# Performance work log

Measured on AMD Instinct MI355X. Metric: run time of the kernel, lower is better.

The kernel has to match this reference:

```python
import jax, jax.numpy as jnp
import numpy as np
import math

EMBED = 1024
HEADS = 16
HEAD_DIM = EMBED // HEADS


def setup_inputs() -> dict:
    key = jax.random.key(0)
    ks = jax.random.split(key, 6)
    scale = 1.0 / math.sqrt(EMBED)
    x = jax.random.normal(ks[0], (4, 2048, EMBED), dtype=jnp.float32)
    Wv = jax.random.normal(ks[1], (EMBED, EMBED), dtype=jnp.float32) * scale
    Wk = jax.random.normal(ks[2], (EMBED, EMBED), dtype=jnp.float32) * scale
    Wq = jax.random.normal(ks[3], (EMBED, EMBED), dtype=jnp.float32) * scale
    Wo = jax.random.normal(ks[4], (EMBED, EMBED), dtype=jnp.float32) * scale
    bo = jax.random.normal(ks[5], (EMBED,), dtype=jnp.float32) * 0.02
    return {"x": x, "Wq": Wq, "Wk": Wk, "Wv": Wv, "Wo": Wo, "bo": bo}


def reference(x, Wq, Wk, Wv, Wo, bo):
    N, S, E = x.shape
    H, D = HEADS, HEAD_DIM
    # Linear(E,E,bias=False): y = x @ W.T ; weights here stored as [out,in]
    q = (x @ Wq.T).reshape(N, S, H, D)
    k = (x @ Wk.T).reshape(N, S, H, D)
    v = (x @ Wv.T).reshape(N, S, H, D)
    energy = jnp.einsum('nqhd,nkhd->nhqk', q, k)  # [N,H,S,S]
    attn = jax.nn.softmax(energy / math.sqrt(D), axis=-1)
    out = jnp.einsum('nhql,nlhd->nqhd', attn, v).reshape(N, S, E)
    return out @ Wo.T + bo
```

## Files before the change

kernel.cpp:

```cpp
#include <hip/hip_runtime.h>
#include <stdint.h>

#define NB   4
#define SLEN 2048
#define EMB  1024
#define NH   16
#define HD   64
#define MTOT (NB * SLEN)

typedef __bf16 bf8_t  __attribute__((ext_vector_type(8)));
typedef __bf16 bf4_t  __attribute__((ext_vector_type(4)));
typedef float  f4_t   __attribute__((ext_vector_type(4)));
typedef unsigned int u32x2 __attribute__((ext_vector_type(2)));
typedef unsigned int u32x4 __attribute__((ext_vector_type(4)));

#if __has_builtin(__builtin_amdgcn_exp2f)
#define EXP2(x) __builtin_amdgcn_exp2f(x)
#else
#define EXP2(x) exp2f(x)
#endif

__device__ __forceinline__ void gld16(const void* g, void* l) {
    __builtin_amdgcn_global_load_lds(
        (__attribute__((address_space(1))) void*)(g),
        (__attribute__((address_space(3))) void*)(l),
        16, 0, 0);
}

__device__ __forceinline__ uint32_t pack_bf16_rtn(float a, float b) {
    uint32_t ua = __builtin_bit_cast(uint32_t, a) + 0x8000u;
    uint32_t ub = __builtin_bit_cast(uint32_t, b) + 0x8000u;
    return __builtin_amdgcn_perm(ub, ua, 0x07060302u);
}
__device__ __forceinline__ uint32_t pack_bf16_rtz(float a, float b) {
    return __builtin_amdgcn_perm(__builtin_bit_cast(uint32_t, b),
                                 __builtin_bit_cast(uint32_t, a), 0x07060302u);
}

__global__ __launch_bounds__(256) void cast_all(const float* __restrict__ x,
                                                const float* __restrict__ Wq,
                                                const float* __restrict__ Wk,
                                                const float* __restrict__ Wv,
                                                const float* __restrict__ Wo,
                                                __bf16* __restrict__ xb,
                                                __bf16* __restrict__ wb) {
    int b = blockIdx.x;
    const float* s;
    __bf16* d;
    if (b < 8192) {
        s = x; d = xb;
    } else {
        int y = (b - 8192) >> 10;
        s = (y == 0) ? Wq : (y == 1) ? Wk : (y == 2) ? Wv : Wo;
        d = wb + (size_t)y * (EMB * EMB);
        b = (b - 8192) & 1023;
    }
    int i = (b * 256 + (int)threadIdx.x) * 4;
    float4 f = *(const float4*)(s + i);
    bf4_t o = { (__bf16)f.x, (__bf16)f.y, (__bf16)f.z, (__bf16)f.w };
    *(bf4_t*)(d + i) = o;
}

__device__ __forceinline__ void gstage(const __bf16* __restrict__ A,
                                       const __bf16* __restrict__ B,
                                       int m0, int n0, int k0, int K, int tid,
                                       __bf16* __restrict__ As,
                                       __bf16* __restrict__ Bs) {
#pragma unroll
    for (int t = 0; t < 4; ++t) {
        int c   = t * 256 + tid;
        int row = c >> 3;
        int kc  = (c & 7) ^ (row & 7);
        int cb  = c & ~63;
        gld16(A + (size_t)(m0 + row) * K + k0 + kc * 8, As + cb * 8);
        gld16(B + (size_t)(n0 + row) * K + k0 + kc * 8, Bs + cb * 8);
    }
}

template <bool SWAP>
__device__ __forceinline__ void gcompute(const __bf16* __restrict__ As,
                                         const __bf16* __restrict__ Bs,
                                         f4_t (*acc)[4],
                                         int wm, int wn, int quad, int l16) {
#pragma unroll
    for (int ks = 0; ks < 2; ++ks) {
        bf8_t af[4], bfr[4];
#pragma unroll
        for (int i = 0; i < 4; ++i) {
            int r = wm + i * 16 + l16;
            af[i] = *(const bf8_t*)&As[r * 64 + (((ks * 4 + quad) ^ (r & 7)) * 8)];
        }
#pragma unroll
        for (int j = 0; j < 4; ++j) {
            int r = wn + j * 16 + l16;
            bfr[j] = *(const bf8_t*)&Bs[r * 64 + (((ks * 4 + quad) ^ (r & 7)) * 8)];
        }
#pragma unroll
        for (int i = 0; i < 4; ++i)
#pragma unroll
            for (int j = 0; j < 4; ++j) {
                if (SWAP)
                    acc[i][j] = __builtin_amdgcn_mfma_f32_16x16x32_bf16(
                        bfr[j], af[i], acc[i][j], 0, 0, 0);
                else
                    acc[i][j] = __builtin_amdgcn_mfma_f32_16x16x32_bf16(
                        af[i], bfr[j], acc[i][j], 0, 0, 0);
            }
    }
}

template <bool SWAP>
__device__ __forceinline__ void gkloop(const __bf16* __restrict__ A,
                                       const __bf16* __restrict__ B,
                                       int m0, int n0, int K, int tid,
                                       __bf16* As0, __bf16* Bs0,
                                       __bf16* As1, __bf16* Bs1,
                                       f4_t (*acc)[4],
                                       int wm, int wn, int quad, int l16) {
    gstage(A, B, m0, n0, 0, K, tid, As0, Bs0);
    for (int k0 = 0; k0 < K; k0 += 128) {
        __syncthreads();
        gstage(A, B, m0, n0, k0 + 64, K, tid, As1, Bs1);
        gcompute<SWAP>(As0, Bs0, acc, wm, wn, quad, l16);
        __syncthreads();
        int knn = (k0 + 128 < K) ? k0 + 128 : k0 + 64;
        gstage(A, B, m0, n0, knn, K, tid, As0, Bs0);
        gcompute<SWAP>(As1, Bs1, acc, wm, wn, quad, l16);
    }
}

__global__ __launch_bounds__(256, 2) void proj_qkv(const __bf16* __restrict__ A,
                                                   const __bf16* __restrict__ B,
                                                   __bf16* __restrict__ qb) {
    __shared__ __bf16 As0[128 * 64], Bs0[128 * 64];
    __shared__ __bf16 As1[128 * 64], Bs1[128 * 64];

    const int tid  = threadIdx.x;
    const int lane = tid & 63;
    const int w    = tid >> 6;
    const int quad = lane >> 4;
    const int l16  = lane & 15;
    const int m0   = blockIdx.x * 128;
    const int n0   = blockIdx.y * 128;
    const int wm   = (w >> 1) * 64;
    const int wn   = (w & 1) * 64;

    f4_t acc[4][4];
#pragma unroll
    for (int i = 0; i < 4; ++i)
#pragma unroll
        for (int j = 0; j < 4; ++j) acc[i][j] = (f4_t){0.f, 0.f, 0.f, 0.f};

    if (n0 < 2048) {
        gkloop<true>(A, B, m0, n0, EMB, tid, As0, Bs0, As1, Bs1, acc, wm, wn, quad, l16);
#pragma unroll
        for (int i = 0; i < 4; ++i)
#pragma unroll
            for (int j = 0; j < 4; ++j) {
                int m   = m0 + wm + i * 16 + l16;
                int col = n0 + wn + j * 16 + quad * 4;
                __bf16* dst = (col < 1024) ? qb : qb + (size_t)8 * 1024 * 1024;
                bf4_t pk = { (__bf16)acc[i][j][0], (__bf16)acc[i][j][1],
                             (__bf16)acc[i][j][2], (__bf16)acc[i][j][3] };
                *(bf4_t*)&dst[(size_t)m * 1024 + (col & 1023)] = pk;
            }
    } else {
        gkloop<false>(A, B, m0, n0, EMB, tid, As0, Bs0, As1, Bs1, acc, wm, wn, quad, l16);
        __bf16* vtb = qb + (size_t)16 * 1024 * 1024;
#pragma unroll
        for (int i = 0; i < 4; ++i)
#pragma unroll
            for (int j = 0; j < 4; ++j) {
                int m  = m0 + wm + i * 16 + quad * 4;
                int ch = n0 - 2048 + wn + j * 16 + l16;
                size_t idx = ((size_t)(m >> 11) * 1024 + ch) * 2048 + (m & 2047);
                bf4_t pk = { (__bf16)acc[i][j][0], (__bf16)acc[i][j][1],
                             (__bf16)acc[i][j][2], (__bf16)acc[i][j][3] };
                *(bf4_t*)&vtb[idx] = pk;
            }
    }
}

__global__ __launch_bounds__(256, 2) void gemm_out(const __bf16* __restrict__ A,
                                                   const __bf16* __restrict__ B,
                                                   float* __restrict__ C,
                                                   const float* __restrict__ bias) {
    __shared__ __bf16 As0[128 * 64], Bs0[128 * 64];
    __shared__ __bf16 As1[128 * 64], Bs1[128 * 64];

    const int tid  = threadIdx.x;
    const int lane = tid & 63;
    const int w    = tid >> 6;
    const int quad = lane >> 4;
    const int l16  = lane & 15;
    const int m0   = blockIdx.x * 128;
    const int n0   = blockIdx.y * 128;
    const int wm   = (w >> 1) * 64;
    const int wn   = (w & 1) * 64;

    f4_t acc[4][4];
#pragma unroll
    for (int i = 0; i < 4; ++i)
#pragma unroll
        for (int j = 0; j < 4; ++j) acc[i][j] = (f4_t){0.f, 0.f, 0.f, 0.f};

    gkloop<true>(A, B, m0, n0, EMB, tid, As0, Bs0, As1, Bs1, acc, wm, wn, quad, l16);

#pragma unroll
    for (int i = 0; i < 4; ++i)
#pragma unroll
        for (int j = 0; j < 4; ++j) {
            int m   = m0 + wm + i * 16 + l16;
            int col = n0 + wn + j * 16 + quad * 4;
            float4 bv = *(const float4*)&bias[col];
            float4 ov = { acc[i][j][0] + bv.x, acc[i][j][1] + bv.y,
                          acc[i][j][2] + bv.z, acc[i][j][3] + bv.w };
            *(float4*)&C[(size_t)m * EMB + col] = ov;
        }
}

__device__ __forceinline__ void attn_stage(const __bf16* __restrict__ kbase,
                                           const __bf16* __restrict__ vbase,
                                           int l0, int tid,
                                           __bf16* __restrict__ Ksb,
                                           __bf16* __restrict__ Vsb) {
    int c   = tid;
    int row = c >> 3;
    int kc  = (c & 7) ^ (row & 7);
    int cb  = c & ~63;
    gld16(kbase + (size_t)(l0 + row) * EMB + kc * 8, Ksb + cb * 8);
    gld16(vbase + (size_t)row * SLEN + l0 + kc * 8, Vsb + cb * 8);
}

__device__ __forceinline__ void attn_tile(const __bf16* __restrict__ Ksb,
                                          const __bf16* __restrict__ Vsb,
                                          const bf8_t (*bq)[2], bf8_t aones,
                                          f4_t* ls, f4_t (*o)[4],
                                          int quad, int l16, int sw) {
#pragma unroll
    for (int ks = 0; ks < 2; ++ks) {
        uint32_t pk[2][4];
#pragma unroll
        for (int jkl = 0; jkl < 2; ++jkl) {
            const int jk = ks * 2 + jkl;
            bf8_t ak0 = *(const bf8_t*)&Ksb[(jk * 16 + l16) * 64 + ((quad ^ sw) * 8)];
            bf8_t ak1 = *(const bf8_t*)&Ksb[(jk * 16 + l16) * 64 + (((4 + quad) ^ sw) * 8)];
#pragma unroll
            for (int jq = 0; jq < 2; ++jq) {
                f4_t e = (f4_t){0.f, 0.f, 0.f, 0.f};
                e = __builtin_amdgcn_mfma_f32_16x16x32_bf16(ak0, bq[jq][0], e, 0, 0, 0);
                e = __builtin_amdgcn_mfma_f32_16x16x32_bf16(ak1, bq[jq][1], e, 0, 0, 0);
                pk[jq][jkl * 2 + 0] = pack_bf16_rtz(EXP2(e[0]), EXP2(e[1]));
                pk[jq][jkl * 2 + 1] = pack_bf16_rtz(EXP2(e[2]), EXP2(e[3]));
            }
        }
        bf8_t bp[2];
#pragma unroll
        for (int jq = 0; jq < 2; ++jq) {
            u32x2 s0 = __builtin_amdgcn_permlane32_swap(pk[jq][0], pk[jq][2], false, false);
            u32x2 s1 = __builtin_amdgcn_permlane32_swap(pk[jq][1], pk[jq][3], false, false);
            u32x2 t0 = __builtin_amdgcn_permlane16_swap(s0[0], s0[1], false, false);
            u32x2 t1 = __builtin_amdgcn_permlane16_swap(s1[0], s1[1], false, false);
            bp[jq] = __builtin_bit_cast(bf8_t, (u32x4){t0[0], t1[0], t0[1], t1[1]});
        }
#pragma unroll
        for (int jq = 0; jq < 2; ++jq)
            ls[jq] = __builtin_amdgcn_mfma_f32_16x16x32_bf16(aones, bp[jq], ls[jq], 0, 0, 0);
#pragma unroll
        for (int jd = 0; jd < 4; ++jd) {
            bf8_t av = *(const bf8_t*)&Vsb[(jd * 16 + l16) * 64 +
                                           (((ks * 4 + quad) ^ sw) * 8)];
#pragma unroll
            for (int jq = 0; jq < 2; ++jq)
                o[jq][jd] = __builtin_amdgcn_mfma_f32_16x16x32_bf16(av, bp[jq],
                                                                    o[jq][jd], 0, 0, 0);
        }
    }
}

__global__ __launch_bounds__(512, 4) void attn_fwd(const __bf16* __restrict__ Q,
                                                   const __bf16* __restrict__ K,
                                                   const __bf16* __restrict__ Vt,
                                                   __bf16* __restrict__ O) {
    __shared__ __bf16 Ks0[64 * 64];
    __shared__ __bf16 Ks1[64 * 64];
    __shared__ __bf16 Vs0[64 * 64];
    __shared__ __bf16 Vs1[64 * 64];

    const int tid  = threadIdx.x;
    const int lane = tid & 63;
    const int w    = tid >> 6;
    const int quad = lane >> 4;
    const int l16  = lane & 15;
    const int nh   = blockIdx.x;
    const int n    = nh >> 4;
    const int h    = nh & 15;
    const int q0   = blockIdx.y * 256 + w * 32;

    const float QSCALE = 0.125f * 1.44269504f;

    bf8_t bq[2][2];
#pragma unroll
    for (int jq = 0; jq < 2; ++jq)
#pragma unroll
        for (int ks = 0; ks < 2; ++ks) {
            bf8_t v = *(const bf8_t*)(Q + (size_t)(n * SLEN + q0 + jq * 16 + l16) * EMB +
                                      h * HD + ks * 32 + quad * 8);
#pragma unroll
            for (int t = 0; t < 8; ++t) v[t] = (__bf16)((float)v[t] * QSCALE);
            bq[jq][ks] = v;
        }

    bf8_t aones;
#pragma unroll
    for (int t = 0; t < 8; ++t) aones[t] = (__bf16)1.0f;

    f4_t ls[2];
    f4_t o[2][4];
#pragma unroll
    for (int jq = 0; jq < 2; ++jq) {
        ls[jq] = (f4_t){0.f, 0.f, 0.f, 0.f};
#pragma unroll
        for (int jd = 0; jd < 4; ++jd) o[jq][jd] = (f4_t){0.f, 0.f, 0.f, 0.f};
    }

    const __bf16* kbase = K + (size_t)n * SLEN * EMB + h * HD;
    const __bf16* vbase = Vt + (size_t)nh * HD * SLEN;
    const int sw = l16 & 7;

    attn_stage(kbase, vbase, 0, tid, Ks0, Vs0);

    for (int it = 0; it < 32; it += 2) {
        int l0 = it * 64;
        __syncthreads();
        attn_stage(kbase, vbase, l0 + 64, tid, Ks1, Vs1);
        attn_tile(Ks0, Vs0, bq, aones, ls, o, quad, l16, sw);
        __syncthreads();
        int lnn = (l0 + 128 < SLEN) ? l0 + 128 : l0 + 64;
        attn_stage(kbase, vbase, lnn, tid, Ks0, Vs0);
        attn_tile(Ks1, Vs1, bq, aones, ls, o, quad, l16, sw);
    }

#pragma unroll
    for (int jq = 0; jq < 2; ++jq) {
        float inv = 1.0f / ls[jq][0];
#pragma unroll
        for (int jd = 0; jd < 4; ++jd) {
            uint32_t d0 = pack_bf16_rtn(o[jq][jd][0] * inv, o[jq][jd][1] * inv);
            uint32_t d1 = pack_bf16_rtn(o[jq][jd][2] * inv, o[jq][jd][3] * inv);
            *(uint2*)&O[(size_t)(n * SLEN + q0 + jq * 16 + l16) * EMB + h * HD +
                        jd * 16 + quad * 4] = (uint2){d0, d1};
        }
    }
}

extern "C" void kernel_launch(void* const* d_in, const int* in_sizes, int n_in,
                              void* d_out, int out_size, void* d_ws, size_t ws_size,
                              hipStream_t stream) {
    const float* x  = (const float*)d_in[0];
    const float* Wq = (const float*)d_in[1];
    const float* Wk = (const float*)d_in[2];
    const float* Wv = (const float*)d_in[3];
    const float* Wo = (const float*)d_in[4];
    const float* bo = (const float*)d_in[5];

    char* wsb = (char*)d_ws;
    const size_t MB = (size_t)1 << 20;
    __bf16* xb  = (__bf16*)(wsb + 0 * MB);
    __bf16* ab  = xb;
    __bf16* wqb = (__bf16*)(wsb + 16 * MB);
    __bf16* wob = (__bf16*)(wsb + 22 * MB);
    __bf16* qb  = (__bf16*)(wsb + 24 * MB);
    __bf16* kb  = (__bf16*)(wsb + 40 * MB);
    __bf16* vtb = (__bf16*)(wsb + 56 * MB);

    cast_all<<<dim3(12288), dim3(256), 0, stream>>>(x, Wq, Wk, Wv, Wo, xb, wqb);

    proj_qkv<<<dim3(MTOT / 128, 3072 / 128), 256, 0, stream>>>(xb, wqb, qb);

    attn_fwd<<<dim3(NB * NH, SLEN / 256), 512, 0, stream>>>(qb, kb, vtb, ab);

    gemm_out<<<dim3(MTOT / 128, EMB / 128), 256, 0, stream>>>(ab, wob, (float*)d_out, bo);
}
```

Measured before the change: 241.4 us.

## Software-pipeline QK-exp and PV across paired KV tiles with double-sized stages

The attention inner loop now processes two 64-key tiles per stage and interleaves the QK/exp computation of the next half-tile with the PV MFMAs of the previous one. The goal is to hide exp/permlane latency behind matrix work. PV MFMAs run at raised wave priority via s_setprio. Shared memory doubles to four K/V buffers, which lowers how many blocks fit per CU and raises register pressure from the extra live pk arrays. The final prefetch wraps back to tile 0 to avoid an out-of-range load.

```diff
diff --git a/kernel.cpp b/kernel.cpp
--- a/kernel.cpp
+++ b/kernel.cpp
@@ -232,60 +232,81 @@
     gld16(vbase + (size_t)row * SLEN + l0 + kc * 8, Vsb + cb * 8);
 }
 
-__device__ __forceinline__ void attn_tile(const __bf16* __restrict__ Ksb,
-                                          const __bf16* __restrict__ Vsb,
+__device__ __forceinline__ void qkexp_half(const __bf16* __restrict__ Ksb, int ks,
+                                           const bf8_t (*bq)[2],
+                                           uint32_t (*pk)[4],
+                                           int quad, int l16, int sw) {
+#pragma unroll
+    for (int jkl = 0; jkl < 2; ++jkl) {
+        const int jk = ks * 2 + jkl;
+        bf8_t ak0 = *(const bf8_t*)&Ksb[(jk * 16 + l16) * 64 + ((quad ^ sw) * 8)];
+        bf8_t ak1 = *(const bf8_t*)&Ksb[(jk * 16 + l16) * 64 + (((4 + quad) ^ sw) * 8)];
+#pragma unroll
+        for (int jq = 0; jq < 2; ++jq) {
+            f4_t e = (f4_t){0.f, 0.f, 0.f, 0.f};
+            e = __builtin_amdgcn_mfma_f32_16x16x32_bf16(ak0, bq[jq][0], e, 0, 0, 0);
+            e = __builtin_amdgcn_mfma_f32_16x16x32_bf16(ak1, bq[jq][1], e, 0, 0, 0);
+            pk[jq][jkl * 2 + 0] = pack_bf16_rtz(EXP2(e[0]), EXP2(e[1]));
+            pk[jq][jkl * 2 + 1] = pack_bf16_rtz(EXP2(e[2]), EXP2(e[3]));
+        }
+    }
+}
+
+__device__ __forceinline__ void pv_half(const __bf16* __restrict__ Vsb, int ks,
+                                        const uint32_t (*pk)[4], bf8_t aones,
+                                        f4_t* ls, f4_t (*o)[4],
+                                        int quad, int l16, int sw) {
+    bf8_t bp[2];
+#pragma unroll
+    for (int jq = 0; jq < 2; ++jq) {
+        u32x2 s0 = __builtin_amdgcn_permlane32_swap(pk[jq][0], pk[jq][2], false, false);
+        u32x2 s1 = __builtin_amdgcn_permlane32_swap(pk[jq][1], pk[jq][3], false, false);
+        u32x2 t0 = __builtin_amdgcn_permlane16_swap(s0[0], s0[1], false, false);
+        u32x2 t1 = __builtin_amdgcn_permlane16_swap(s1[0], s1[1], false, false);
+        bp[jq] = __builtin_bit_cast(bf8_t, (u32x4){t0[0], t1[0], t0[1], t1[1]});
+    }
+    __builtin_amdgcn_s_setprio(1);
+#pragma unroll
+    for (int jq = 0; jq < 2; ++jq)
+        ls[jq] = __builtin_amdgcn_mfma_f32_16x16x32_bf16(aones, bp[jq], ls[jq], 0, 0, 0);
+#pragma unroll
+    for (int jd = 0; jd < 4; ++jd) {
+        bf8_t av = *(const bf8_t*)&Vsb[(jd * 16 + l16) * 64 +
+                                       (((ks * 4 + quad) ^ sw) * 8)];
+#pragma unroll
+        for (int jq = 0; jq < 2; ++jq)
+            o[jq][jd] = __builtin_amdgcn_mfma_f32_16x16x32_bf16(av, bp[jq],
+                                                                o[jq][jd], 0, 0, 0);
+    }
+    __builtin_amdgcn_s_setprio(0);
+}
+
+__device__ __forceinline__ void attn_pair(const __bf16* __restrict__ Ka,
+                                          const __bf16* __restrict__ Kb,
+                                          const __bf16* __restrict__ Va,
+                                          const __bf16* __restrict__ Vb,
                                           const bf8_t (*bq)[2], bf8_t aones,
                                           f4_t* ls, f4_t (*o)[4],
                                           int quad, int l16, int sw) {
-#pragma unroll
-    for (int ks = 0; ks < 2; ++ks) {
-        uint32_t pk[2][4];
-#pragma unroll
-        for (int jkl = 0; jkl < 2; ++jkl) {
-            const int jk = ks * 2 + jkl;
-            bf8_t ak0 = *(const bf8_t*)&Ksb[(jk * 16 + l16) * 64 + ((quad ^ sw) * 8)];
-            bf8_t ak1 = *(const bf8_t*)&Ksb[(jk * 16 + l16) * 64 + (((4 + quad) ^ sw) * 8)];
-#pragma unroll
-            for (int jq = 0; jq < 2; ++jq) {
-                f4_t e = (f4_t){0.f, 0.f, 0.f, 0.f};
-                e = __builtin_amdgcn_mfma_f32_16x16x32_bf16(ak0, bq[jq][0], e, 0, 0, 0);
-                e = __builtin_amdgcn_mfma_f32_16x16x32_bf16(ak1, bq[jq][1], e, 0, 0, 0);
-                pk[jq][jkl * 2 + 0] = pack_bf16_rtz(EXP2(e[0]), EXP2(e[1]));
-                pk[jq][jkl * 2 + 1] = pack_bf16_rtz(EXP2(e[2]), EXP2(e[3]));
-            }
-        }
-        bf8_t bp[2];
-#pragma unroll
-        for (int jq = 0; jq < 2; ++jq) {
-            u32x2 s0 = __builtin_amdgcn_permlane32_swap(pk[jq][0], pk[jq][2], false, false);
-            u32x2 s1 = __builtin_amdgcn_permlane32_swap(pk[jq][1], pk[jq][3], false, false);
-            u32x2 t0 = __builtin_amdgcn_permlane16_swap(s0[0], s0[1], false, false);
-            u32x2 t1 = __builtin_amdgcn_permlane16_swap(s1[0], s1[1], false, false);
-            bp[jq] = __builtin_bit_cast(bf8_t, (u32x4){t0[0], t1[0], t0[1], t1[1]});
-        }
-#pragma unroll
-        for (int jq = 0; jq < 2; ++jq)
-            ls[jq] = __builtin_amdgcn_mfma_f32_16x16x32_bf16(aones, bp[jq], ls[jq], 0, 0, 0);
-#pragma unroll
-        for (int jd = 0; jd < 4; ++jd) {
-            bf8_t av = *(const bf8_t*)&Vsb[(jd * 16 + l16) * 64 +
-                                           (((ks * 4 + quad) ^ sw) * 8)];
-#pragma unroll
-            for (int jq = 0; jq < 2; ++jq)
-                o[jq][jd] = __builtin_amdgcn_mfma_f32_16x16x32_bf16(av, bp[jq],
-                                                                    o[jq][jd], 0, 0, 0);
-        }
-    }
+    uint32_t pkA[2][4], pkB[2][4];
+    qkexp_half(Ka, 0, bq, pkA, quad, l16, sw);
+    qkexp_half(Ka, 1, bq, pkB, quad, l16, sw);
+    pv_half(Va, 0, pkA, aones, ls, o, quad, l16, sw);
+    qkexp_half(Kb, 0, bq, pkA, quad, l16, sw);
+    pv_half(Va, 1, pkB, aones, ls, o, quad, l16, sw);
+    qkexp_half(Kb, 1, bq, pkB, quad, l16, sw);
+    pv_half(Vb, 0, pkA, aones, ls, o, quad, l16, sw);
+    pv_half(Vb, 1, pkB, aones, ls, o, quad, l16, sw);
 }
 
 __global__ __launch_bounds__(512, 4) void attn_fwd(const __bf16* __restrict__ Q,
                                                    const __bf16* __restrict__ K,
                                                    const __bf16* __restrict__ Vt,
                                                    __bf16* __restrict__ O) {
-    __shared__ __bf16 Ks0[64 * 64];
-    __shared__ __bf16 Ks1[64 * 64];
-    __shared__ __bf16 Vs0[64 * 64];
-    __shared__ __bf16 Vs1[64 * 64];
+    __shared__ __bf16 Ks0[64 * 64], Ks1[64 * 64];
+    __shared__ __bf16 Ks2[64 * 64], Ks3[64 * 64];
+    __shared__ __bf16 Vs0[64 * 64], Vs1[64 * 64];
+    __shared__ __bf16 Vs2[64 * 64], Vs3[64 * 64];
 
     const int tid  = threadIdx.x;
     const int lane = tid & 63;
@@ -329,16 +350,19 @@
     const int sw = l16 & 7;
 
     attn_stage(kbase, vbase, 0, tid, Ks0, Vs0);
-
-    for (int it = 0; it < 32; it += 2) {
-        int l0 = it * 64;
+    attn_stage(kbase, vbase, 64, tid, Ks1, Vs1);
+
+    for (int it = 0; it < 16; it += 2) {
+        int L = it * 128;
         __syncthreads();
-        attn_stage(kbase, vbase, l0 + 64, tid, Ks1, Vs1);
-        attn_tile(Ks0, Vs0, bq, aones, ls, o, quad, l16, sw);
+        attn_stage(kbase, vbase, L + 128, tid, Ks2, Vs2);
+        attn_stage(kbase, vbase, L + 192, tid, Ks3, Vs3);
+        attn_pair(Ks0, Ks1, Vs0, Vs1, bq, aones, ls, o, quad, l16, sw);
         __syncthreads();
-        int lnn = (l0 + 128 < SLEN) ? l0 + 128 : l0 + 64;
-        attn_stage(kbase, vbase, lnn, tid, Ks0, Vs0);
-        attn_tile(Ks1, Vs1, bq, aones, ls, o, quad, l16, sw);
+        int Lnn = (it + 2 < 16) ? L + 256 : 0;
+        attn_stage(kbase, vbase, Lnn, tid, Ks0, Vs0);
+        attn_stage(kbase, vbase, Lnn + 64, tid, Ks1, Vs1);
+        attn_pair(Ks2, Ks3, Vs2, Vs3, bq, aones, ls, o, quad, l16, sw);
     }
 
 #pragma unroll
```

New measurement: 242.7 us. No clear change (+0.5%).
